# Kernel optimization log

Hardware: AMD Instinct MI355X
Metric: run time of the kernel (lower is better)

Reference implementation:

```python
import jax, jax.numpy as jnp
import numpy as np

GRID_SIZE = 5
SPLINE_ORDER = 3

def _grid(in_features, dtype):
    # efficient-KAN default grid over [-1, 1], extended by spline_order knots each side
    h = 2.0 / GRID_SIZE
    g = jnp.arange(-SPLINE_ORDER, GRID_SIZE + SPLINE_ORDER + 1, dtype=dtype) * h - 1.0
    return jnp.broadcast_to(g, (in_features, g.shape[0]))  # (in, G+2k+1)

def _b_splines(x, grid):
    # x: (..., in) -> bases: (..., in, G+k) via Cox-de Boor recursion
    xk = x[..., None]
    bases = ((xk >= grid[:, :-1]) & (xk < grid[:, 1:])).astype(x.dtype)
    for k in range(1, SPLINE_ORDER + 1):
        left = (xk - grid[:, :-(k + 1)]) / (grid[:, k:-1] - grid[:, :-(k + 1)]) * bases[..., :-1]
        right = (grid[:, k + 1:] - xk) / (grid[:, k + 1:] - grid[:, 1:-k]) * bases[..., 1:]
        bases = left + right
    return bases

def _kan_linear(x, base_w, spline_w, scaler):
    # base branch: SiLU(x) @ W_base^T ; spline branch: einsum over B-spline basis
    grid = _grid(base_w.shape[1], x.dtype)
    bases = _b_splines(x, grid)                      # (..., in, G+k)
    scaled = spline_w * scaler[..., None]            # (out, in, G+k)
    base_out = jax.nn.silu(x) @ base_w.T
    spline_out = jnp.einsum('...ig,oig->...o', bases, scaled)
    return base_out + spline_out

def setup_inputs() -> dict:
    key = jax.random.key(0)
    ks = jax.random.split(key, 11)
    B, N, C, O = 2, 256, 64, 64
    GK = GRID_SIZE + SPLINE_ORDER
    return {
        'x': jax.random.normal(ks[0], (B, N, C), jnp.float32),
        'adj': jax.random.randint(ks[1], (B, N, N), 0, 2, jnp.int32),
        'fw_base': jax.random.normal(ks[2], (1, C), jnp.float32) * 0.1,
        'fw_spline': jax.random.normal(ks[3], (1, C, GK), jnp.float32) * 0.1,
        'fw_scaler': jax.random.normal(ks[4], (1, C), jnp.float32) * 0.1,
        'mw_base': jax.random.normal(ks[5], (O, C), jnp.float32) * 0.1,
        'mw_spline': jax.random.normal(ks[6], (O, C, GK), jnp.float32) * 0.1,
        'mw_scaler': jax.random.normal(ks[7], (O, C), jnp.float32) * 0.1,
        'uw_base': jax.random.normal(ks[8], (O, C + O), jnp.float32) * 0.1,
        'uw_spline': jax.random.normal(ks[9], (O, C + O, GK), jnp.float32) * 0.1,
        'uw_scaler': jax.random.normal(ks[10], (O, C + O), jnp.float32) * 0.1,
    }

def reference(x, adj, fw_base, fw_spline, fw_scaler, mw_base, mw_spline, mw_scaler, uw_base, uw_spline, uw_scaler):
    # r_ij = h_i - h_j : (B, N, N, C)
    r_ij = x[:, :, None, :] - x[:, None, :, :]
    energy = _kan_linear(r_ij, fw_base, fw_spline, fw_scaler)[..., 0]  # (B, N, N)
    energy = jnp.where(adj == 0, jnp.asarray(-1e9, energy.dtype), energy)
    alpha = jax.nn.softmax(energy, axis=-1)
    msg_val = _kan_linear(x, mw_base, mw_spline, mw_scaler)            # (B, N, O)
    aggr = jnp.einsum('bij,bjo->bio', alpha, msg_val)
    combined = jnp.concatenate([x, aggr], axis=-1)
    return _kan_linear(combined, uw_base, uw_spline, uw_scaler)
```

## Files before the change

kernel.cpp:

```cpp
#include <hip/hip_runtime.h>
#include <math.h>

#define NB 256
#define CH 64
#define OUTF 64
#define GK 8
#define UIN 128
#define KM (CH * 9)
#define KM4 (KM / 4)
#define KU (UIN * 9)
#define KU4 (KU / 4)

#define WS_MSG 0
#define WS_XT 32768
#define WS_W2M 65536
#define WS_W2U 102400

__device__ __forceinline__ float silu(float v) {
    return v * __builtin_amdgcn_rcpf(1.0f + __expf(-v));
}

__device__ __forceinline__ void spline4(float r, int& d, float4& v) {
    float p = (r + 2.2f) * 2.5f;
    float fd = floorf(p);
    d = (int)fd;
    float u = p - fd;
    if ((unsigned)d > 10u) d = 11;
    float um = 1.0f - u;
    float u2 = u * u, u3 = u2 * u;
    const float k6 = 1.0f / 6.0f;
    v.x = um * um * um * k6;
    v.y = (3.0f * u3 - 6.0f * u2 + 4.0f) * k6;
    v.z = (-3.0f * u3 + 3.0f * u2 + 3.0f * u + 1.0f) * k6;
    v.w = u3 * k6;
}

__global__ __launch_bounds__(256) void prep_kernel(
    const float* __restrict__ x,
    const float* __restrict__ mwb, const float* __restrict__ mws,
    const float* __restrict__ mwsc,
    const float* __restrict__ uwb, const float* __restrict__ uws,
    const float* __restrict__ uwsc,
    float* __restrict__ ws) {
    int t = blockIdx.x * 256 + threadIdx.x;
    if (t < 2 * NB * CH) {
        int b = t >> 14, rem = t & 16383, j = rem >> 6, c = rem & 63;
        ws[WS_XT + b * CH * NB + c * NB + j] = x[t];
        return;
    }
    int t2 = t - 2 * NB * CH;
    if (t2 < KM4 * OUTF) {
        int k4 = t2 >> 6, o = t2 & 63;
        float4 v;
#pragma unroll
        for (int kk = 0; kk < 4; ++kk) {
            int k = k4 * 4 + kk, c = k / 9, g = k - c * 9;
            ((float*)&v)[kk] = (g < 8)
                ? mws[(o * CH + c) * GK + g] * mwsc[o * CH + c]
                : mwb[o * CH + c];
        }
        ((float4*)(ws + WS_W2M))[t2] = v;
        return;
    }
    int t3 = t2 - KM4 * OUTF;
    if (t3 < KU4 * OUTF) {
        int k4 = t3 >> 6, o = t3 & 63;
        float4 v;
#pragma unroll
        for (int kk = 0; kk < 4; ++kk) {
            int k = k4 * 4 + kk, c = k / 9, g = k - c * 9;
            ((float*)&v)[kk] = (g < 8)
                ? uws[(o * UIN + c) * GK + g] * uwsc[o * UIN + c]
                : uwb[o * UIN + c];
        }
        ((float4*)(ws + WS_W2U))[t3] = v;
    }
}

__global__ __launch_bounds__(256) void msg_kernel(
    const float* __restrict__ x, const float* __restrict__ w2m,
    float* __restrict__ msg) {
    const int row = blockIdx.x, tid = threadIdx.x;
    __shared__ __align__(16) float F[KM];
    __shared__ float part[4][OUTF];

    if (tid < CH) {
        float v = x[row * CH + tid];
#pragma unroll
        for (int g = 0; g < 8; ++g) F[tid * 9 + g] = 0.0f;
        F[tid * 9 + 8] = silu(v);
        int d; float4 vv; spline4(v, d, vv);
#pragma unroll
        for (int k = 0; k < 4; ++k) {
            int m = d - 3 + k;
            if ((unsigned)m < 8u) F[tid * 9 + m] = ((const float*)&vv)[k];
        }
    }
    __syncthreads();

    const int o = tid & 63, w = tid >> 6;
    const float4* W = (const float4*)w2m;
    const float4* Fv = (const float4*)F;
    float acc = 0.0f;
#pragma unroll 4
    for (int k4 = w * 36; k4 < w * 36 + 36; ++k4) {
        float4 f = Fv[k4];
        float4 wt = W[k4 * 64 + o];
        acc += f.x * wt.x + f.y * wt.y + f.z * wt.z + f.w * wt.w;
    }
    part[w][o] = acc;
    __syncthreads();
    if (tid < OUTF)
        msg[row * OUTF + tid] =
            part[0][tid] + part[1][tid] + part[2][tid] + part[3][tid];
}

__global__ __launch_bounds__(256) void gat_kernel(
    const float* __restrict__ xT,
    const float* __restrict__ x,
    const int* __restrict__ adj,
    const float* __restrict__ fwb, const float* __restrict__ fws,
    const float* __restrict__ fwsc,
    const float* __restrict__ w2u,
    const float* __restrict__ msg,
    float* __restrict__ out) {
    const int b = blockIdx.x >> 8;
    const int i = blockIdx.x & 255;
    const int tid = threadIdx.x;

    __shared__ float4 cpad[CH][16];
    __shared__ float2 xisf[CH];
    __shared__ float alpha[NB];
    __shared__ float comb[UIN];
    __shared__ __align__(16) float Fu[KU];
    __shared__ float part[4][OUTF];
    __shared__ float wred[4];

    if (tid < CH) {
        float v = x[(b * NB + i) * CH + tid];
        xisf[tid] = make_float2(v, fwb[tid]);
        comb[tid] = v;
    }
#pragma unroll
    for (int e = tid; e < CH * 16; e += 256) {
        int c = e >> 4, dd = e & 15;
        float4 cf = make_float4(0.f, 0.f, 0.f, 0.f);
        if (dd <= 10) {
            float sc = fwsc[c];
            float w0 = 0.f, w1 = 0.f, w2 = 0.f, w3 = 0.f;
            int m0 = dd - 3;
            if ((unsigned)(m0 + 0) < 8u) w0 = fws[c * GK + m0 + 0] * sc;
            if ((unsigned)(m0 + 1) < 8u) w1 = fws[c * GK + m0 + 1] * sc;
            if ((unsigned)(m0 + 2) < 8u) w2 = fws[c * GK + m0 + 2] * sc;
            if ((unsigned)(m0 + 3) < 8u) w3 = fws[c * GK + m0 + 3] * sc;
            cf.x = (w0 + 4.0f * w1 + w2) * (1.0f / 6.0f);
            cf.y = (w2 - w0) * 0.5f;
            cf.z = (w0 - 2.0f * w1 + w2) * 0.5f;
            cf.w = (w3 - w0 + 3.0f * (w1 - w2)) * (1.0f / 6.0f);
        }
        cpad[c][dd] = cf;
    }
    __syncthreads();

    const float* xTb = xT + b * CH * NB;
    float e = 0.0f;
#pragma unroll 4
    for (int c = 0; c < CH; ++c) {
        float xj = xTb[c * NB + tid];
        float2 xs = xisf[c];
        float r = xs.x - xj;
        float pp = (r + 2.2f) * 2.5f;
        float fd = floorf(pp);
        int d = (int)fd;
        float u = pp - fd;
        if ((unsigned)d > 10u) d = 11;
        float4 cf = cpad[c][d];
        e += cf.x + u * (cf.y + u * (cf.z + u * cf.w)) + silu(r) * xs.y;
    }
    if (adj[(b * NB + i) * NB + tid] == 0) e = -1e9f;

    float mx = e;
#pragma unroll
    for (int off = 32; off > 0; off >>= 1)
        mx = fmaxf(mx, __shfl_xor(mx, off, 64));
    if ((tid & 63) == 0) wred[tid >> 6] = mx;
    __syncthreads();
    mx = fmaxf(fmaxf(wred[0], wred[1]), fmaxf(wred[2], wred[3]));
    float pexp = __expf(e - mx);
    float sw = pexp;
#pragma unroll
    for (int off = 32; off > 0; off >>= 1)
        sw += __shfl_xor(sw, off, 64);
    __syncthreads();
    if ((tid & 63) == 0) wred[tid >> 6] = sw;
    __syncthreads();
    float denom = wred[0] + wred[1] + wred[2] + wred[3];
    alpha[tid] = pexp * __builtin_amdgcn_rcpf(denom);
    __syncthreads();

    {
        const int o = tid & 63, seg = tid >> 6;
        const float* msgb = msg + (b * NB + seg * 64) * OUTF;
        float a = 0.0f;
#pragma unroll 8
        for (int jj = 0; jj < 64; ++jj)
            a += alpha[seg * 64 + jj] * msgb[jj * OUTF + o];
        part[seg][o] = a;
    }
    __syncthreads();
    if (tid < OUTF)
        comb[CH + tid] = part[0][tid] + part[1][tid] + part[2][tid] + part[3][tid];
    __syncthreads();

    if (tid < UIN) {
        float v = comb[tid];
#pragma unroll
        for (int g = 0; g < 8; ++g) Fu[tid * 9 + g] = 0.0f;
        Fu[tid * 9 + 8] = silu(v);
        int d; float4 vv; spline4(v, d, vv);
#pragma unroll
        for (int k = 0; k < 4; ++k) {
            int m = d - 3 + k;
            if ((unsigned)m < 8u) Fu[tid * 9 + m] = ((const float*)&vv)[k];
        }
    }
    __syncthreads();

    {
        const int o = tid & 63, w = tid >> 6;
        const float4* W = (const float4*)w2u;
        const float4* Fv = (const float4*)Fu;
        float acc = 0.0f;
#pragma unroll 4
        for (int k4 = w * 72; k4 < w * 72 + 72; ++k4) {
            float4 f = Fv[k4];
            float4 wt = W[k4 * 64 + o];
            acc += f.x * wt.x + f.y * wt.y + f.z * wt.z + f.w * wt.w;
        }
        part[w][o] = acc;
    }
    __syncthreads();
    if (tid < OUTF)
        out[(b * NB + i) * OUTF + tid] =
            part[0][tid] + part[1][tid] + part[2][tid] + part[3][tid];
}

extern "C" void kernel_launch(void* const* d_in, const int* in_sizes, int n_in,
                              void* d_out, int out_size, void* d_ws, size_t ws_size,
                              hipStream_t stream) {
    const float* x     = (const float*)d_in[0];
    const int*   adj   = (const int*)d_in[1];
    const float* fwb   = (const float*)d_in[2];
    const float* fws   = (const float*)d_in[3];
    const float* fwsc  = (const float*)d_in[4];
    const float* mwb   = (const float*)d_in[5];
    const float* mws   = (const float*)d_in[6];
    const float* mwsc  = (const float*)d_in[7];
    const float* uwb   = (const float*)d_in[8];
    const float* uws   = (const float*)d_in[9];
    const float* uwsc  = (const float*)d_in[10];
    float* out = (float*)d_out;
    float* ws = (float*)d_ws;

    const int BN = in_sizes[0] / CH;

    const int prep_threads = 2 * NB * CH + KM4 * OUTF + KU4 * OUTF;
    prep_kernel<<<(prep_threads + 255) / 256, 256, 0, stream>>>(
        x, mwb, mws, mwsc, uwb, uws, uwsc, ws);
    msg_kernel<<<BN, 256, 0, stream>>>(x, ws + WS_W2M, ws + WS_MSG);
    gat_kernel<<<BN, 256, 0, stream>>>(ws + WS_XT, x, adj, fwb, fws, fwsc,
                                       ws + WS_W2U, ws + WS_MSG, out);
}
```

Before: 99.97 us.

## Fuse prep, message and attention kernels into one cooperative kernel with grid syncs

Merges the three launches into a single cooperative kernel with 512 blocks that uses grid-wide barriers between the prep, message and attention phases. The x transpose now goes through a shared-memory tile, and the attention spline coefficient table is built once in workspace instead of in every block. Phases share one union of shared memory. This removes two kernel launch gaps in exchange for grid-sync cost and the constraints of a cooperative launch.

```diff
diff --git a/kernel.cpp b/kernel.cpp
--- a/kernel.cpp
+++ b/kernel.cpp
@@ -1,5 +1,8 @@
 #include <hip/hip_runtime.h>
+#include <hip/hip_cooperative_groups.h>
 #include <math.h>
+
+namespace cg = cooperative_groups;
 
 #define NB 256
 #define CH 64
@@ -15,6 +18,7 @@
 #define WS_XT 32768
 #define WS_W2M 65536
 #define WS_W2U 102400
+#define WS_CPAD 176128
 
 __device__ __forceinline__ float silu(float v) {
     return v * __builtin_amdgcn_rcpf(1.0f + __expf(-v));
@@ -35,146 +39,149 @@
     v.w = u3 * k6;
 }
 
-__global__ __launch_bounds__(256) void prep_kernel(
-    const float* __restrict__ x,
+__global__ __launch_bounds__(256, 2) void fused_kernel(
+    const float* __restrict__ x, const int* __restrict__ adj,
+    const float* __restrict__ fwb, const float* __restrict__ fws,
+    const float* __restrict__ fwsc,
     const float* __restrict__ mwb, const float* __restrict__ mws,
     const float* __restrict__ mwsc,
     const float* __restrict__ uwb, const float* __restrict__ uws,
     const float* __restrict__ uwsc,
-    float* __restrict__ ws) {
-    int t = blockIdx.x * 256 + threadIdx.x;
-    if (t < 2 * NB * CH) {
-        int b = t >> 14, rem = t & 16383, j = rem >> 6, c = rem & 63;
-        ws[WS_XT + b * CH * NB + c * NB + j] = x[t];
-        return;
-    }
-    int t2 = t - 2 * NB * CH;
-    if (t2 < KM4 * OUTF) {
-        int k4 = t2 >> 6, o = t2 & 63;
-        float4 v;
-#pragma unroll
-        for (int kk = 0; kk < 4; ++kk) {
-            int k = k4 * 4 + kk, c = k / 9, g = k - c * 9;
-            ((float*)&v)[kk] = (g < 8)
-                ? mws[(o * CH + c) * GK + g] * mwsc[o * CH + c]
-                : mwb[o * CH + c];
-        }
-        ((float4*)(ws + WS_W2M))[t2] = v;
-        return;
-    }
-    int t3 = t2 - KM4 * OUTF;
-    if (t3 < KU4 * OUTF) {
-        int k4 = t3 >> 6, o = t3 & 63;
-        float4 v;
-#pragma unroll
-        for (int kk = 0; kk < 4; ++kk) {
-            int k = k4 * 4 + kk, c = k / 9, g = k - c * 9;
-            ((float*)&v)[kk] = (g < 8)
-                ? uws[(o * UIN + c) * GK + g] * uwsc[o * UIN + c]
-                : uwb[o * UIN + c];
-        }
-        ((float4*)(ws + WS_W2U))[t3] = v;
-    }
-}
-
-__global__ __launch_bounds__(256) void msg_kernel(
-    const float* __restrict__ x, const float* __restrict__ w2m,
-    float* __restrict__ msg) {
-    const int row = blockIdx.x, tid = threadIdx.x;
-    __shared__ __align__(16) float F[KM];
-    __shared__ float part[4][OUTF];
-
-    if (tid < CH) {
-        float v = x[row * CH + tid];
-#pragma unroll
-        for (int g = 0; g < 8; ++g) F[tid * 9 + g] = 0.0f;
-        F[tid * 9 + 8] = silu(v);
-        int d; float4 vv; spline4(v, d, vv);
-#pragma unroll
-        for (int k = 0; k < 4; ++k) {
-            int m = d - 3 + k;
-            if ((unsigned)m < 8u) F[tid * 9 + m] = ((const float*)&vv)[k];
-        }
-    }
-    __syncthreads();
-
-    const int o = tid & 63, w = tid >> 6;
-    const float4* W = (const float4*)w2m;
-    const float4* Fv = (const float4*)F;
-    float acc = 0.0f;
+    float* __restrict__ ws, float* __restrict__ out) {
+    const int blk = blockIdx.x, tid = threadIdx.x;
+    cg::grid_group grid = cg::this_grid();
+
+    __shared__ union {
+        struct { float tile[64][65]; } ta;
+        struct { __align__(16) float F[KM]; float part[4][OUTF]; } mb;
+        struct {
+            float4 cpad[CH][16];
+            float2 xisf[CH];
+            float alpha[NB];
+            float comb[UIN];
+            __align__(16) float Fu[KU];
+            float part[4][OUTF];
+            float wred[4];
+        } gc;
+    } sm;
+
+    float* msg  = ws + WS_MSG;
+    float* xT   = ws + WS_XT;
+    float* w2m  = ws + WS_W2M;
+    float* w2u  = ws + WS_W2U;
+    float* cpws = ws + WS_CPAD;
+
+    if (blk < 8) {
+        const int b = blk >> 2, jt = blk & 3;
+#pragma unroll
+        for (int it = 0; it < 16; ++it) {
+            int idx = it * 256 + tid, jj = idx >> 6, cc = idx & 63;
+            sm.ta.tile[jj][cc] = x[(b * NB + jt * 64 + jj) * CH + cc];
+        }
+        __syncthreads();
+#pragma unroll
+        for (int it = 0; it < 16; ++it) {
+            int idx = it * 256 + tid, cc = idx >> 6, jj = idx & 63;
+            xT[b * CH * NB + cc * NB + jt * 64 + jj] = sm.ta.tile[jj][cc];
+        }
+    } else if (blk < 8 + KM4) {
+        const int k4 = blk - 8, o = tid >> 2, kk = tid & 3;
+        int k = k4 * 4 + kk, c = k / 9, g = k - c * 9;
+        float v = (g < 8) ? mws[(o * CH + c) * GK + g] * mwsc[o * CH + c]
+                          : mwb[o * CH + c];
+        w2m[(k4 * 64 + o) * 4 + kk] = v;
+    } else if (blk < 8 + KM4 + KU4) {
+        const int k4 = blk - 8 - KM4, o = tid >> 2, kk = tid & 3;
+        int k = k4 * 4 + kk, c = k / 9, g = k - c * 9;
+        float v = (g < 8) ? uws[(o * UIN + c) * GK + g] * uwsc[o * UIN + c]
+                          : uwb[o * UIN + c];
+        w2u[(k4 * 64 + o) * 4 + kk] = v;
+    } else if (blk == 8 + KM4 + KU4) {
+        for (int e = tid; e < CH * 16; e += 256) {
+            int c = e >> 4, dd = e & 15;
+            float4 cf = make_float4(0.f, 0.f, 0.f, 0.f);
+            if (dd <= 10) {
+                float sc = fwsc[c];
+                float w0 = 0.f, w1 = 0.f, w2 = 0.f, w3 = 0.f;
+                int m0 = dd - 3;
+                if ((unsigned)(m0 + 0) < 8u) w0 = fws[c * GK + m0 + 0] * sc;
+                if ((unsigned)(m0 + 1) < 8u) w1 = fws[c * GK + m0 + 1] * sc;
+                if ((unsigned)(m0 + 2) < 8u) w2 = fws[c * GK + m0 + 2] * sc;
+                if ((unsigned)(m0 + 3) < 8u) w3 = fws[c * GK + m0 + 3] * sc;
+                cf.x = (w0 + 4.0f * w1 + w2) * (1.0f / 6.0f);
+                cf.y = (w2 - w0) * 0.5f;
+                cf.z = (w0 - 2.0f * w1 + w2) * 0.5f;
+                cf.w = (w3 - w0 + 3.0f * (w1 - w2)) * (1.0f / 6.0f);
+            }
+            ((float4*)cpws)[e] = cf;
+        }
+    }
+
+    grid.sync();
+
+    {
+        const int row = blk;
+        if (tid < CH) {
+            float v = x[row * CH + tid];
+#pragma unroll
+            for (int g = 0; g < 8; ++g) sm.mb.F[tid * 9 + g] = 0.0f;
+            sm.mb.F[tid * 9 + 8] = silu(v);
+            int d; float4 vv; spline4(v, d, vv);
+#pragma unroll
+            for (int k = 0; k < 4; ++k) {
+                int m = d - 3 + k;
+                if ((unsigned)m < 8u) sm.mb.F[tid * 9 + m] = ((const float*)&vv)[k];
+            }
+        }
+        __syncthreads();
+
+        const int o = tid & 63, w = tid >> 6;
+        const float4* W = (const float4*)w2m;
+        const float4* Fv = (const float4*)sm.mb.F;
+        float acc = 0.0f;
 #pragma unroll 4
-    for (int k4 = w * 36; k4 < w * 36 + 36; ++k4) {
-        float4 f = Fv[k4];
-        float4 wt = W[k4 * 64 + o];
-        acc += f.x * wt.x + f.y * wt.y + f.z * wt.z + f.w * wt.w;
-    }
-    part[w][o] = acc;
-    __syncthreads();
-    if (tid < OUTF)
-        msg[row * OUTF + tid] =
-            part[0][tid] + part[1][tid] + part[2][tid] + part[3][tid];
-}
-
-__global__ __launch_bounds__(256) void gat_kernel(
-    const float* __restrict__ xT,
-    const float* __restrict__ x,
-    const int* __restrict__ adj,
-    const float* __restrict__ fwb, const float* __restrict__ fws,
-    const float* __restrict__ fwsc,
-    const float* __restrict__ w2u,
-    const float* __restrict__ msg,
-    float* __restrict__ out) {
-    const int b = blockIdx.x >> 8;
-    const int i = blockIdx.x & 255;
-    const int tid = threadIdx.x;
-
-    __shared__ float4 cpad[CH][16];
-    __shared__ float2 xisf[CH];
-    __shared__ float alpha[NB];
-    __shared__ float comb[UIN];
-    __shared__ __align__(16) float Fu[KU];
-    __shared__ float part[4][OUTF];
-    __shared__ float wred[4];
-
+        for (int k4 = w * 36; k4 < w * 36 + 36; ++k4) {
+            float4 f = Fv[k4];
+            float4 wt = W[k4 * 64 + o];
+            acc += f.x * wt.x + f.y * wt.y + f.z * wt.z + f.w * wt.w;
+        }
+        sm.mb.part[w][o] = acc;
+        __syncthreads();
+        if (tid < OUTF)
+            msg[row * OUTF + tid] = sm.mb.part[0][tid] + sm.mb.part[1][tid]
+                                  + sm.mb.part[2][tid] + sm.mb.part[3][tid];
+    }
+
+    grid.sync();
+
+    const int b = blk >> 8, i = blk & 255;
+
+    {
+        const float4* cp = (const float4*)cpws;
+        float4* dst = &sm.gc.cpad[0][0];
+#pragma unroll
+        for (int e = tid; e < CH * 16; e += 256) dst[e] = cp[e];
+    }
     if (tid < CH) {
         float v = x[(b * NB + i) * CH + tid];
-        xisf[tid] = make_float2(v, fwb[tid]);
-        comb[tid] = v;
-    }
-#pragma unroll
-    for (int e = tid; e < CH * 16; e += 256) {
-        int c = e >> 4, dd = e & 15;
-        float4 cf = make_float4(0.f, 0.f, 0.f, 0.f);
-        if (dd <= 10) {
-            float sc = fwsc[c];
-            float w0 = 0.f, w1 = 0.f, w2 = 0.f, w3 = 0.f;
-            int m0 = dd - 3;
-            if ((unsigned)(m0 + 0) < 8u) w0 = fws[c * GK + m0 + 0] * sc;
-            if ((unsigned)(m0 + 1) < 8u) w1 = fws[c * GK + m0 + 1] * sc;
-            if ((unsigned)(m0 + 2) < 8u) w2 = fws[c * GK + m0 + 2] * sc;
-            if ((unsigned)(m0 + 3) < 8u) w3 = fws[c * GK + m0 + 3] * sc;
-            cf.x = (w0 + 4.0f * w1 + w2) * (1.0f / 6.0f);
-            cf.y = (w2 - w0) * 0.5f;
-            cf.z = (w0 - 2.0f * w1 + w2) * 0.5f;
-            cf.w = (w3 - w0 + 3.0f * (w1 - w2)) * (1.0f / 6.0f);
-        }
-        cpad[c][dd] = cf;
+        sm.gc.xisf[tid] = make_float2(v, fwb[tid]);
+        sm.gc.comb[tid] = v;
     }
     __syncthreads();
 
     const float* xTb = xT + b * CH * NB;
     float e = 0.0f;
-#pragma unroll 4
+#pragma unroll 8
     for (int c = 0; c < CH; ++c) {
         float xj = xTb[c * NB + tid];
-        float2 xs = xisf[c];
+        float2 xs = sm.gc.xisf[c];
         float r = xs.x - xj;
         float pp = (r + 2.2f) * 2.5f;
         float fd = floorf(pp);
         int d = (int)fd;
         float u = pp - fd;
         if ((unsigned)d > 10u) d = 11;
-        float4 cf = cpad[c][d];
+        float4 cf = sm.gc.cpad[c][d];
         e += cf.x + u * (cf.y + u * (cf.z + u * cf.w)) + silu(r) * xs.y;
     }
     if (adj[(b * NB + i) * NB + tid] == 0) e = -1e9f;
@@ -183,19 +190,20 @@
 #pragma unroll
     for (int off = 32; off > 0; off >>= 1)
         mx = fmaxf(mx, __shfl_xor(mx, off, 64));
-    if ((tid & 63) == 0) wred[tid >> 6] = mx;
-    __syncthreads();
-    mx = fmaxf(fmaxf(wred[0], wred[1]), fmaxf(wred[2], wred[3]));
+    if ((tid & 63) == 0) sm.gc.wred[tid >> 6] = mx;
+    __syncthreads();
+    mx = fmaxf(fmaxf(sm.gc.wred[0], sm.gc.wred[1]),
+               fmaxf(sm.gc.wred[2], sm.gc.wred[3]));
     float pexp = __expf(e - mx);
     float sw = pexp;
 #pragma unroll
     for (int off = 32; off > 0; off >>= 1)
         sw += __shfl_xor(sw, off, 64);
     __syncthreads();
-    if ((tid & 63) == 0) wred[tid >> 6] = sw;
-    __syncthreads();
-    float denom = wred[0] + wred[1] + wred[2] + wred[3];
-    alpha[tid] = pexp * __builtin_amdgcn_rcpf(denom);
+    if ((tid & 63) == 0) sm.gc.wred[tid >> 6] = sw;
+    __syncthreads();
+    float denom = sm.gc.wred[0] + sm.gc.wred[1] + sm.gc.wred[2] + sm.gc.wred[3];
+    sm.gc.alpha[tid] = pexp * __builtin_amdgcn_rcpf(denom);
     __syncthreads();
 
     {
@@ -204,24 +212,25 @@
         float a = 0.0f;
 #pragma unroll 8
         for (int jj = 0; jj < 64; ++jj)
-            a += alpha[seg * 64 + jj] * msgb[jj * OUTF + o];
-        part[seg][o] = a;
+            a += sm.gc.alpha[seg * 64 + jj] * msgb[jj * OUTF + o];
+        sm.gc.part[seg][o] = a;
     }
     __syncthreads();
     if (tid < OUTF)
-        comb[CH + tid] = part[0][tid] + part[1][tid] + part[2][tid] + part[3][tid];
+        sm.gc.comb[CH + tid] = sm.gc.part[0][tid] + sm.gc.part[1][tid]
+                             + sm.gc.part[2][tid] + sm.gc.part[3][tid];
     __syncthreads();
 
     if (tid < UIN) {
-        float v = comb[tid];
-#pragma unroll
-        for (int g = 0; g < 8; ++g) Fu[tid * 9 + g] = 0.0f;
-        Fu[tid * 9 + 8] = silu(v);
+        float v = sm.gc.comb[tid];
+#pragma unroll
+        for (int g = 0; g < 8; ++g) sm.gc.Fu[tid * 9 + g] = 0.0f;
+        sm.gc.Fu[tid * 9 + 8] = silu(v);
         int d; float4 vv; spline4(v, d, vv);
 #pragma unroll
         for (int k = 0; k < 4; ++k) {
             int m = d - 3 + k;
-            if ((unsigned)m < 8u) Fu[tid * 9 + m] = ((const float*)&vv)[k];
+            if ((unsigned)m < 8u) sm.gc.Fu[tid * 9 + m] = ((const float*)&vv)[k];
         }
     }
     __syncthreads();
@@ -229,7 +238,7 @@
     {
         const int o = tid & 63, w = tid >> 6;
         const float4* W = (const float4*)w2u;
-        const float4* Fv = (const float4*)Fu;
+        const float4* Fv = (const float4*)sm.gc.Fu;
         float acc = 0.0f;
 #pragma unroll 4
         for (int k4 = w * 72; k4 < w * 72 + 72; ++k4) {
@@ -237,12 +246,13 @@
             float4 wt = W[k4 * 64 + o];
             acc += f.x * wt.x + f.y * wt.y + f.z * wt.z + f.w * wt.w;
         }
-        part[w][o] = acc;
+        sm.gc.part[w][o] = acc;
     }
     __syncthreads();
     if (tid < OUTF)
         out[(b * NB + i) * OUTF + tid] =
-            part[0][tid] + part[1][tid] + part[2][tid] + part[3][tid];
+            sm.gc.part[0][tid] + sm.gc.part[1][tid]
+          + sm.gc.part[2][tid] + sm.gc.part[3][tid];
 }
 
 extern "C" void kernel_launch(void* const* d_in, const int* in_sizes, int n_in,
@@ -262,12 +272,12 @@
     float* out = (float*)d_out;
     float* ws = (float*)d_ws;
 
-    const int BN = in_sizes[0] / CH;
-
-    const int prep_threads = 2 * NB * CH + KM4 * OUTF + KU4 * OUTF;
-    prep_kernel<<<(prep_threads + 255) / 256, 256, 0, stream>>>(
-        x, mwb, mws, mwsc, uwb, uws, uwsc, ws);
-    msg_kernel<<<BN, 256, 0, stream>>>(x, ws + WS_W2M, ws + WS_MSG);
-    gat_kernel<<<BN, 256, 0, stream>>>(ws + WS_XT, x, adj, fwb, fws, fwsc,
-                                       ws + WS_W2U, ws + WS_MSG, out);
-}
+    void* args[] = {
+        (void*)&x, (void*)&adj, (void*)&fwb, (void*)&fws, (void*)&fwsc,
+        (void*)&mwb, (void*)&mws, (void*)&mwsc,
+        (void*)&uwb, (void*)&uws, (void*)&uwsc,
+        (void*)&ws, (void*)&out
+    };
+    hipLaunchCooperativeKernel((const void*)fused_kernel,
+                               dim3(512), dim3(256), args, 0, stream);
+}
```

Result: slower. 234.5 us (+134.5%).

## Drop prep kernel; read spline weights directly and precompute energy coefficients once

Applied to the files above, without the earlier changes.

Removes the prep kernel that transposed x and repacked the message/update weights into an interleaved layout. The message and update layers now read the original spline, scaler and base weights directly and apply the scaler after the per-channel dot product. The feature-energy cubic coefficient table is built once by an extra block in the message kernel instead of by every attention block. The attention loop reads x rows as float4 instead of a transposed copy. This saves one launch and the repacking traffic, but each thread now makes strided per-thread weight loads (rows of 8 floats per output) that coalesce worse, and every thread reads x rows 256 bytes apart.

```diff
diff --git a/kernel.cpp b/kernel.cpp
--- a/kernel.cpp
+++ b/kernel.cpp
@@ -6,15 +6,9 @@
 #define OUTF 64
 #define GK 8
 #define UIN 128
-#define KM (CH * 9)
-#define KM4 (KM / 4)
-#define KU (UIN * 9)
-#define KU4 (KU / 4)
 
 #define WS_MSG 0
-#define WS_XT 32768
-#define WS_W2M 65536
-#define WS_W2U 102400
+#define WS_CPAD 32768
 
 __device__ __forceinline__ float silu(float v) {
     return v * __builtin_amdgcn_rcpf(1.0f + __expf(-v));
@@ -35,94 +29,88 @@
     v.w = u3 * k6;
 }
 
-__global__ __launch_bounds__(256) void prep_kernel(
+__device__ __forceinline__ void build_basis(float v, float* row8, float* sil) {
+    int d; float4 vv; spline4(v, d, vv);
+#pragma unroll
+    for (int g = 0; g < 8; ++g) row8[g] = 0.0f;
+#pragma unroll
+    for (int k = 0; k < 4; ++k) {
+        int m = d - 3 + k;
+        if ((unsigned)m < 8u) row8[m] = ((const float*)&vv)[k];
+    }
+    *sil = silu(v);
+}
+
+__global__ __launch_bounds__(256, 2) void msg_kernel(
     const float* __restrict__ x,
+    const float* __restrict__ fws, const float* __restrict__ fwsc,
     const float* __restrict__ mwb, const float* __restrict__ mws,
     const float* __restrict__ mwsc,
+    float* __restrict__ ws) {
+    const int blk = blockIdx.x, tid = threadIdx.x;
+
+    if (blk == 512) {
+        for (int e = tid; e < CH * 16; e += 256) {
+            int c = e >> 4, dd = e & 15;
+            float4 cf = make_float4(0.f, 0.f, 0.f, 0.f);
+            if (dd <= 10) {
+                float sc = fwsc[c];
+                float w0 = 0.f, w1 = 0.f, w2 = 0.f, w3 = 0.f;
+                int m0 = dd - 3;
+                if ((unsigned)(m0 + 0) < 8u) w0 = fws[c * GK + m0 + 0] * sc;
+                if ((unsigned)(m0 + 1) < 8u) w1 = fws[c * GK + m0 + 1] * sc;
+                if ((unsigned)(m0 + 2) < 8u) w2 = fws[c * GK + m0 + 2] * sc;
+                if ((unsigned)(m0 + 3) < 8u) w3 = fws[c * GK + m0 + 3] * sc;
+                cf.x = (w0 + 4.0f * w1 + w2) * (1.0f / 6.0f);
+                cf.y = (w2 - w0) * 0.5f;
+                cf.z = (w0 - 2.0f * w1 + w2) * 0.5f;
+                cf.w = (w3 - w0 + 3.0f * (w1 - w2)) * (1.0f / 6.0f);
+            }
+            ((float4*)(ws + WS_CPAD))[e] = cf;
+        }
+        return;
+    }
+
+    const int row = blk;
+    __shared__ __align__(16) float Mb[CH][8];
+    __shared__ float Msil[CH];
+    __shared__ float part[4][OUTF];
+
+    if (tid < CH)
+        build_basis(x[row * CH + tid], Mb[tid], &Msil[tid]);
+    __syncthreads();
+
+    const int o = tid & 63, w = tid >> 6;
+    const int c0 = w * 16;
+    float acc = 0.0f;
+#pragma unroll
+    for (int cc = 0; cc < 16; cc += 4) {
+        float4 sc4 = *(const float4*)&mwsc[o * CH + c0 + cc];
+        float4 bw4 = *(const float4*)&mwb[o * CH + c0 + cc];
+#pragma unroll
+        for (int t = 0; t < 4; ++t) {
+            int c = c0 + cc + t;
+            const float4* wp = (const float4*)&mws[(o * CH + c) * GK];
+            float4 wa = wp[0], wb = wp[1];
+            const float* B = Mb[c];
+            float s = B[0]*wa.x + B[1]*wa.y + B[2]*wa.z + B[3]*wa.w
+                    + B[4]*wb.x + B[5]*wb.y + B[6]*wb.z + B[7]*wb.w;
+            acc += s * ((const float*)&sc4)[t] + Msil[c] * ((const float*)&bw4)[t];
+        }
+    }
+    part[w][o] = acc;
+    __syncthreads();
+    if (tid < OUTF)
+        ws[WS_MSG + row * OUTF + tid] =
+            part[0][tid] + part[1][tid] + part[2][tid] + part[3][tid];
+}
+
+__global__ __launch_bounds__(256, 2) void gat_kernel(
+    const float* __restrict__ x, const int* __restrict__ adj,
+    const float* __restrict__ fwb,
     const float* __restrict__ uwb, const float* __restrict__ uws,
     const float* __restrict__ uwsc,
-    float* __restrict__ ws) {
-    int t = blockIdx.x * 256 + threadIdx.x;
-    if (t < 2 * NB * CH) {
-        int b = t >> 14, rem = t & 16383, j = rem >> 6, c = rem & 63;
-        ws[WS_XT + b * CH * NB + c * NB + j] = x[t];
-        return;
-    }
-    int t2 = t - 2 * NB * CH;
-    if (t2 < KM4 * OUTF) {
-        int k4 = t2 >> 6, o = t2 & 63;
-        float4 v;
-#pragma unroll
-        for (int kk = 0; kk < 4; ++kk) {
-            int k = k4 * 4 + kk, c = k / 9, g = k - c * 9;
-            ((float*)&v)[kk] = (g < 8)
-                ? mws[(o * CH + c) * GK + g] * mwsc[o * CH + c]
-                : mwb[o * CH + c];
-        }
-        ((float4*)(ws + WS_W2M))[t2] = v;
-        return;
-    }
-    int t3 = t2 - KM4 * OUTF;
-    if (t3 < KU4 * OUTF) {
-        int k4 = t3 >> 6, o = t3 & 63;
-        float4 v;
-#pragma unroll
-        for (int kk = 0; kk < 4; ++kk) {
-            int k = k4 * 4 + kk, c = k / 9, g = k - c * 9;
-            ((float*)&v)[kk] = (g < 8)
-                ? uws[(o * UIN + c) * GK + g] * uwsc[o * UIN + c]
-                : uwb[o * UIN + c];
-        }
-        ((float4*)(ws + WS_W2U))[t3] = v;
-    }
-}
-
-__global__ __launch_bounds__(256) void msg_kernel(
-    const float* __restrict__ x, const float* __restrict__ w2m,
-    float* __restrict__ msg) {
-    const int row = blockIdx.x, tid = threadIdx.x;
-    __shared__ __align__(16) float F[KM];
-    __shared__ float part[4][OUTF];
-
-    if (tid < CH) {
-        float v = x[row * CH + tid];
-#pragma unroll
-        for (int g = 0; g < 8; ++g) F[tid * 9 + g] = 0.0f;
-        F[tid * 9 + 8] = silu(v);
-        int d; float4 vv; spline4(v, d, vv);
-#pragma unroll
-        for (int k = 0; k < 4; ++k) {
-            int m = d - 3 + k;
-            if ((unsigned)m < 8u) F[tid * 9 + m] = ((const float*)&vv)[k];
-        }
-    }
-    __syncthreads();
-
-    const int o = tid & 63, w = tid >> 6;
-    const float4* W = (const float4*)w2m;
-    const float4* Fv = (const float4*)F;
-    float acc = 0.0f;
-#pragma unroll 4
-    for (int k4 = w * 36; k4 < w * 36 + 36; ++k4) {
-        float4 f = Fv[k4];
-        float4 wt = W[k4 * 64 + o];
-        acc += f.x * wt.x + f.y * wt.y + f.z * wt.z + f.w * wt.w;
-    }
-    part[w][o] = acc;
-    __syncthreads();
-    if (tid < OUTF)
-        msg[row * OUTF + tid] =
-            part[0][tid] + part[1][tid] + part[2][tid] + part[3][tid];
-}
-
-__global__ __launch_bounds__(256) void gat_kernel(
-    const float* __restrict__ xT,
-    const float* __restrict__ x,
-    const int* __restrict__ adj,
-    const float* __restrict__ fwb, const float* __restrict__ fws,
-    const float* __restrict__ fwsc,
-    const float* __restrict__ w2u,
-    const float* __restrict__ msg,
+    const float* __restrict__ ws,
     float* __restrict__ out) {
     const int b = blockIdx.x >> 8;
     const int i = blockIdx.x & 255;
@@ -132,50 +120,42 @@
     __shared__ float2 xisf[CH];
     __shared__ float alpha[NB];
     __shared__ float comb[UIN];
-    __shared__ __align__(16) float Fu[KU];
+    __shared__ __align__(16) float Fb[UIN][8];
+    __shared__ float Fsil[UIN];
     __shared__ float part[4][OUTF];
     __shared__ float wred[4];
 
+    {
+        const float4* cp = (const float4*)(ws + WS_CPAD);
+        float4* dst = &cpad[0][0];
+#pragma unroll
+        for (int e = tid; e < CH * 16; e += 256) dst[e] = cp[e];
+    }
     if (tid < CH) {
         float v = x[(b * NB + i) * CH + tid];
         xisf[tid] = make_float2(v, fwb[tid]);
         comb[tid] = v;
     }
-#pragma unroll
-    for (int e = tid; e < CH * 16; e += 256) {
-        int c = e >> 4, dd = e & 15;
-        float4 cf = make_float4(0.f, 0.f, 0.f, 0.f);
-        if (dd <= 10) {
-            float sc = fwsc[c];
-            float w0 = 0.f, w1 = 0.f, w2 = 0.f, w3 = 0.f;
-            int m0 = dd - 3;
-            if ((unsigned)(m0 + 0) < 8u) w0 = fws[c * GK + m0 + 0] * sc;
-            if ((unsigned)(m0 + 1) < 8u) w1 = fws[c * GK + m0 + 1] * sc;
-            if ((unsigned)(m0 + 2) < 8u) w2 = fws[c * GK + m0 + 2] * sc;
-            if ((unsigned)(m0 + 3) < 8u) w3 = fws[c * GK + m0 + 3] * sc;
-            cf.x = (w0 + 4.0f * w1 + w2) * (1.0f / 6.0f);
-            cf.y = (w2 - w0) * 0.5f;
-            cf.z = (w0 - 2.0f * w1 + w2) * 0.5f;
-            cf.w = (w3 - w0 + 3.0f * (w1 - w2)) * (1.0f / 6.0f);
-        }
-        cpad[c][dd] = cf;
-    }
-    __syncthreads();
-
-    const float* xTb = xT + b * CH * NB;
+    __syncthreads();
+
+    const float4* xjp = (const float4*)(x + (b * NB + tid) * CH);
     float e = 0.0f;
 #pragma unroll 4
-    for (int c = 0; c < CH; ++c) {
-        float xj = xTb[c * NB + tid];
-        float2 xs = xisf[c];
-        float r = xs.x - xj;
-        float pp = (r + 2.2f) * 2.5f;
-        float fd = floorf(pp);
-        int d = (int)fd;
-        float u = pp - fd;
-        if ((unsigned)d > 10u) d = 11;
-        float4 cf = cpad[c][d];
-        e += cf.x + u * (cf.y + u * (cf.z + u * cf.w)) + silu(r) * xs.y;
+    for (int q = 0; q < 16; ++q) {
+        float4 xv = xjp[q];
+#pragma unroll
+        for (int t = 0; t < 4; ++t) {
+            int c = q * 4 + t;
+            float2 xs = xisf[c];
+            float r = xs.x - ((const float*)&xv)[t];
+            float pp = (r + 2.2f) * 2.5f;
+            float fd = floorf(pp);
+            int d = (int)fd;
+            float u = pp - fd;
+            if ((unsigned)d > 10u) d = 11;
+            float4 cf = cpad[c][d];
+            e += cf.x + u * (cf.y + u * (cf.z + u * cf.w)) + silu(r) * xs.y;
+        }
     }
     if (adj[(b * NB + i) * NB + tid] == 0) e = -1e9f;
 
@@ -200,7 +180,7 @@
 
     {
         const int o = tid & 63, seg = tid >> 6;
-        const float* msgb = msg + (b * NB + seg * 64) * OUTF;
+        const float* msgb = ws + WS_MSG + (b * NB + seg * 64) * OUTF;
         float a = 0.0f;
 #pragma unroll 8
         for (int jj = 0; jj < 64; ++jj)
@@ -212,30 +192,28 @@
         comb[CH + tid] = part[0][tid] + part[1][tid] + part[2][tid] + part[3][tid];
     __syncthreads();
 
-    if (tid < UIN) {
-        float v = comb[tid];
-#pragma unroll
-        for (int g = 0; g < 8; ++g) Fu[tid * 9 + g] = 0.0f;
-        Fu[tid * 9 + 8] = silu(v);
-        int d; float4 vv; spline4(v, d, vv);
-#pragma unroll
-        for (int k = 0; k < 4; ++k) {
-            int m = d - 3 + k;
-            if ((unsigned)m < 8u) Fu[tid * 9 + m] = ((const float*)&vv)[k];
-        }
-    }
+    if (tid < UIN)
+        build_basis(comb[tid], Fb[tid], &Fsil[tid]);
     __syncthreads();
 
     {
         const int o = tid & 63, w = tid >> 6;
-        const float4* W = (const float4*)w2u;
-        const float4* Fv = (const float4*)Fu;
+        const int c0 = w * 32;
         float acc = 0.0f;
-#pragma unroll 4
-        for (int k4 = w * 72; k4 < w * 72 + 72; ++k4) {
-            float4 f = Fv[k4];
-            float4 wt = W[k4 * 64 + o];
-            acc += f.x * wt.x + f.y * wt.y + f.z * wt.z + f.w * wt.w;
+#pragma unroll
+        for (int cc = 0; cc < 32; cc += 4) {
+            float4 sc4 = *(const float4*)&uwsc[o * UIN + c0 + cc];
+            float4 bw4 = *(const float4*)&uwb[o * UIN + c0 + cc];
+#pragma unroll
+            for (int t = 0; t < 4; ++t) {
+                int c = c0 + cc + t;
+                const float4* wp = (const float4*)&uws[(o * UIN + c) * GK];
+                float4 wa = wp[0], wb = wp[1];
+                const float* B = Fb[c];
+                float s = B[0]*wa.x + B[1]*wa.y + B[2]*wa.z + B[3]*wa.w
+                        + B[4]*wb.x + B[5]*wb.y + B[6]*wb.z + B[7]*wb.w;
+                acc += s * ((const float*)&sc4)[t] + Fsil[c] * ((const float*)&bw4)[t];
+            }
         }
         part[w][o] = acc;
     }
@@ -262,12 +240,6 @@
     float* out = (float*)d_out;
     float* ws = (float*)d_ws;
 
-    const int BN = in_sizes[0] / CH;
-
-    const int prep_threads = 2 * NB * CH + KM4 * OUTF + KU4 * OUTF;
-    prep_kernel<<<(prep_threads + 255) / 256, 256, 0, stream>>>(
-        x, mwb, mws, mwsc, uwb, uws, uwsc, ws);
-    msg_kernel<<<BN, 256, 0, stream>>>(x, ws + WS_W2M, ws + WS_MSG);
-    gat_kernel<<<BN, 256, 0, stream>>>(ws + WS_XT, x, adj, fwb, fws, fwsc,
-                                       ws + WS_W2U, ws + WS_MSG, out);
-}
+    msg_kernel<<<513, 256, 0, stream>>>(x, fws, fwsc, mwb, mws, mwsc, ws);
+    gat_kernel<<<512, 256, 0, stream>>>(x, adj, fwb, uwb, uws, uwsc, ws, out);
+}
```

Measured after the change: 122.8 us. +22.8%, slower.
